# Performance work log

Hardware: AMD Instinct MI355X
Metric: run time of the kernel (lower is better)

## Reference

```python
import jax, jax.numpy as jnp
import numpy as np

D_MODEL = 2048
NUM_HEADS = 16
HEAD_DIM = D_MODEL // NUM_HEADS
SCALE = HEAD_DIM ** 0.5
B, TQ, CACHE_LEN = 4, 1024, 1024


def setup_inputs() -> dict:
    key = jax.random.key(0)
    ks = jax.random.split(key, 13)
    f = jnp.float32
    inp = {
        'query': jax.random.normal(ks[0], (B, TQ, D_MODEL), f),
        'key': jax.random.normal(ks[1], (B, TQ, D_MODEL), f),
        'value': jax.random.normal(ks[2], (B, TQ, D_MODEL), f),
        'cache_key': jax.random.normal(ks[3], (B, CACHE_LEN, D_MODEL), f),
        'cache_value': jax.random.normal(ks[4], (B, CACHE_LEN, D_MODEL), f),
        'Wq': jax.random.normal(ks[5], (D_MODEL, D_MODEL), f) * 0.02,
        'bq': jnp.zeros((D_MODEL,), f),
        'Wk': jax.random.normal(ks[6], (D_MODEL, D_MODEL), f) * 0.02,
        'bk': jnp.zeros((D_MODEL,), f),
        'Wv': jax.random.normal(ks[7], (D_MODEL, D_MODEL), f) * 0.02,
        'bv': jnp.zeros((D_MODEL,), f),
        'Wo': jax.random.normal(ks[8], (D_MODEL, D_MODEL), f) * 0.02,
        'bo': jnp.zeros((D_MODEL,), f),
    }
    return inp


def _split(x):
    b, t, _ = x.shape
    return jnp.transpose(x.reshape(b, t, NUM_HEADS, HEAD_DIM), (0, 2, 1, 3))  # [B,H,T,Dh]


def reference(query, key, value, cache_key, cache_value, Wq, bq, Wk, bk, Wv, bv, Wo, bo):
    b, tq, _ = query.shape
    Q = query @ Wq.T + bq
    K = key @ Wk.T + bk
    V = value @ Wv.T + bv
    # cache holds already-projected K/V; concat along time
    K = jnp.concatenate([cache_key, K], axis=1)
    V = jnp.concatenate([cache_value, V], axis=1)
    total = K.shape[1]
    Qh, Kh, Vh = _split(Q), _split(K), _split(V)  # [B,H,T,Dh]
    scores = jnp.einsum('bhqd,bhkd->bhqk', Qh, Kh) / SCALE  # [B,H,Tq,total]
    # faithful to original: tril(Tq, total) mask (row i sees cols 0..i)
    mask = jnp.tril(jnp.ones((tq, total), dtype=bool))
    scores = jnp.where(mask[None, None], scores, -jnp.inf)
    attn = jax.nn.softmax(scores, axis=-1)  # eval mode: no dropout
    out = jnp.einsum('bhqk,bhkd->bhqd', attn, Vh)
    out = jnp.transpose(out, (0, 2, 1, 3)).reshape(b, tq, D_MODEL)
    out = out @ Wo.T + bo
    # new cache: torch reshapes the transposed [B,H,T,Dh] tensor directly
    new_k = Kh.reshape(b, -1, D_MODEL)
    new_v = Vh.reshape(b, -1, D_MODEL)
    return out, new_k, new_v
```

## Files before the change

### kernel.cpp

```cpp
#include <hip/hip_runtime.h>
#include <hip/hip_bf16.h>


typedef __bf16 bf16x8 __attribute__((ext_vector_type(8)));
typedef __bf16 bf16x4 __attribute__((ext_vector_type(4)));
typedef unsigned short u16x8 __attribute__((ext_vector_type(8)));
typedef float  f32x4  __attribute__((ext_vector_type(4)));
typedef unsigned int u32;

#define MFMA16(a, b, c) __builtin_amdgcn_mfma_f32_16x16x32_bf16((a), (b), (c), 0, 0, 0)

__device__ __forceinline__ void async16(__bf16* lds_p, const __bf16* g) {
    __builtin_amdgcn_global_load_lds(
        (__attribute__((address_space(1))) void*)g,
        (__attribute__((address_space(3))) void*)lds_p, 16, 0, 0);
}

__global__ __launch_bounds__(256) void prep(
    const float* __restrict__ q, const float* __restrict__ k, const float* __restrict__ v,
    const float* __restrict__ wq, const float* __restrict__ wk,
    const float* __restrict__ wv, const float* __restrict__ wo,
    const float* __restrict__ ck, const float* __restrict__ cv,
    float* __restrict__ nk, float* __restrict__ nv,
    __bf16* __restrict__ dq, __bf16* __restrict__ dk, __bf16* __restrict__ dv,
    __bf16* __restrict__ dwq, __bf16* __restrict__ dwk,
    __bf16* __restrict__ dwv, __bf16* __restrict__ dwo,
    __bf16* __restrict__ ckb, __bf16* __restrict__ cvb) {
    const int nthreads = gridDim.x * blockDim.x;
    for (int i = blockIdx.x * blockDim.x + threadIdx.x; i < 9437184; i += nthreads) {
        if (i < 4194304) {
            const int sel = i >> 21;
            const int j = i & 2097151;
            const int dh4 = j & 31;
            const int t = (j >> 5) & 1023;
            const int h = (j >> 15) & 15;
            const int b = j >> 19;
            const float* src = sel ? cv : ck;
            float* dst = sel ? nv : nk;
            __bf16* dstb = sel ? cvb : ckb;
            const size_t si = ((size_t)(b << 10) + t) * 2048 + (h << 7) + (dh4 << 2);
            const size_t di = ((size_t)b << 22) + ((size_t)h << 18) + (t << 7) + (dh4 << 2);
            const size_t bi = (((size_t)(b * 16 + h) * 1024 + t) << 7) + (dh4 << 2);
            const f32x4 x = *(const f32x4*)&src[si];
            *(f32x4*)&dst[di] = x;
            bf16x4 bx;
#pragma unroll
            for (int e = 0; e < 4; e++) bx[e] = (__bf16)x[e];
            *(bf16x4*)&dstb[bi] = bx;
        } else {
            const float* s;
            __bf16* d;
            int off;
            if (i < 7340032) {
                const int ii = i - 4194304;
                const int r = ii >> 20;
                off = ii & 1048575;
                s = (r == 0) ? q : (r == 1) ? k : v;
                d = (r == 0) ? dq : (r == 1) ? dk : dv;
            } else {
                const int ii = i - 7340032;
                const int r = ii >> 19;
                off = ii & 524287;
                s = (r == 0) ? wq : (r == 1) ? wk : (r == 2) ? wv : wo;
                d = (r == 0) ? dwq : (r == 1) ? dwk : (r == 2) ? dwv : dwo;
            }
            const f32x4 x0 = *(const f32x4*)(s + (size_t)off * 8);
            const f32x4 x1 = *(const f32x4*)(s + (size_t)off * 8 + 4);
            bf16x8 o;
#pragma unroll
            for (int j2 = 0; j2 < 4; j2++) {
                o[j2]     = (__bf16)x0[j2];
                o[j2 + 4] = (__bf16)x1[j2];
            }
            *(bf16x8*)(d + (size_t)off * 8) = o;
        }
    }
}

template <int MODE>
__global__ __launch_bounds__(512, 2) void gemm8(
    const __bf16* __restrict__ A,
    const __bf16* __restrict__ W0, const __bf16* __restrict__ W1,
    const __bf16* __restrict__ W2,
    const float* __restrict__ bz0, const float* __restrict__ bz1,
    const float* __restrict__ bz2,
    void* __restrict__ C0, float* __restrict__ C1, float* __restrict__ C2) {
    extern __shared__ __bf16 lds[];
    constexpr int K = 2048;
    const int tid = threadIdx.x;
    const int w = tid >> 6, lane = tid & 63;
    const int wm = w >> 2, wn = w & 3;
    const int g = lane >> 4, c = lane & 15;

    const int lin = blockIdx.x;
    const int nb = lin & 7, mb = lin >> 3;
    const int m0 = mb << 8, n0 = nb << 8;
    const int seg = (MODE == 1) ? (mb >> 4) : 0;
    const __bf16* W = (MODE == 0 || seg == 0) ? W0 : (seg == 1) ? W1 : W2;
    const float* bias = (MODE == 0) ? bz0 : (seg == 0) ? bz0 : (seg == 1) ? bz1 : bz2;

    const __bf16* Ab = A + (size_t)m0 * K;
    const __bf16* Wb = W + (size_t)n0 * K;

    const int sch = (lane & 3) ^ (((lane >> 5) & 1) << 1);
    const int srow = lane >> 2;
    const int foff = c * 32 + ((g ^ ((c >> 3) << 1)) << 3);
    const int arow0 = wm * 8;
    const int brow0 = wn * 4;

    f32x4 acc[8][4] = {};

    auto stg = [&](const __bf16* src, int T, int kk, int region, int bf) {
#pragma unroll
        for (int cc = 0; cc < 2; cc++) {
            const __bf16* gs = src + (size_t)((cc * 8 + w) * 16 + srow) * K
                             + T * 64 + kk * 32 + sch * 8;
            async16(&lds[bf * 32768 + region * 16384 + kk * 8192 + (cc * 8 + w) * 512], gs);
        }
    };

    stg(Ab, 0, 0, 0, 0); stg(Wb, 0, 0, 1, 0);
    stg(Ab, 0, 1, 0, 0); stg(Wb, 0, 1, 1, 0);
    stg(Ab, 1, 0, 0, 1); stg(Wb, 1, 0, 1, 1);
    stg(Ab, 1, 1, 0, 1); stg(Wb, 1, 1, 1, 1);
    asm volatile("s_waitcnt vmcnt(0)" ::: "memory");
    asm volatile("s_barrier" ::: "memory");

#pragma unroll 2
    for (int T = 0; T < 32; T++) {
        const int bf = T & 1;
        const int ab = bf * 32768;
        const int bb = bf * 32768 + 16384;
        bf16x8 fa[4], fb[4], fb2[4];

#pragma unroll
        for (int i = 0; i < 4; i++)
            fa[i] = *(const bf16x8*)&lds[ab + (arow0 + i) * 512 + foff];
#pragma unroll
        for (int j = 0; j < 4; j++)
            fb[j] = *(const bf16x8*)&lds[bb + (brow0 + j) * 512 + foff];
        if (T >= 1 && T <= 30) stg(Ab, T + 1, 1, 0, bf ^ 1);
        asm volatile("s_barrier" ::: "memory");
        asm volatile("s_waitcnt lgkmcnt(0)" ::: "memory");
        __builtin_amdgcn_sched_barrier(0);
        __builtin_amdgcn_s_setprio(1);
#pragma unroll
        for (int i = 0; i < 4; i++)
#pragma unroll
            for (int j = 0; j < 4; j++)
                acc[i][j] = MFMA16(fa[i], fb[j], acc[i][j]);
        __builtin_amdgcn_s_setprio(0);
        asm volatile("s_barrier" ::: "memory");

#pragma unroll
        for (int i = 0; i < 4; i++)
            fa[i] = *(const bf16x8*)&lds[ab + (arow0 + 4 + i) * 512 + foff];
        if (T >= 1 && T <= 30) stg(Wb, T + 1, 1, 1, bf ^ 1);
        asm volatile("s_barrier" ::: "memory");
        asm volatile("s_waitcnt lgkmcnt(0)" ::: "memory");
        __builtin_amdgcn_sched_barrier(0);
        __builtin_amdgcn_s_setprio(1);
#pragma unroll
        for (int i = 0; i < 4; i++)
#pragma unroll
            for (int j = 0; j < 4; j++)
                acc[4 + i][j] = MFMA16(fa[i], fb[j], acc[4 + i][j]);
        __builtin_amdgcn_s_setprio(0);
        asm volatile("s_barrier" ::: "memory");

#pragma unroll
        for (int i = 0; i < 4; i++)
            fa[i] = *(const bf16x8*)&lds[ab + 8192 + (arow0 + i) * 512 + foff];
#pragma unroll
        for (int j = 0; j < 4; j++)
            fb2[j] = *(const bf16x8*)&lds[bb + 8192 + (brow0 + j) * 512 + foff];
        if (T <= 29) stg(Ab, T + 2, 0, 0, bf);
        asm volatile("s_barrier" ::: "memory");
        asm volatile("s_waitcnt lgkmcnt(0)" ::: "memory");
        __builtin_amdgcn_sched_barrier(0);
        __builtin_amdgcn_s_setprio(1);
#pragma unroll
        for (int i = 0; i < 4; i++)
#pragma unroll
            for (int j = 0; j < 4; j++)
                acc[i][j] = MFMA16(fa[i], fb2[j], acc[i][j]);
        __builtin_amdgcn_s_setprio(0);
        asm volatile("s_barrier" ::: "memory");

#pragma unroll
        for (int i = 0; i < 4; i++)
            fa[i] = *(const bf16x8*)&lds[ab + 8192 + (arow0 + 4 + i) * 512 + foff];
        if (T <= 29) stg(Wb, T + 2, 0, 1, bf);
        if (T >= 30) asm volatile("s_waitcnt vmcnt(0)" ::: "memory");
        else         asm volatile("s_waitcnt vmcnt(4)" ::: "memory");
        asm volatile("s_barrier" ::: "memory");
        asm volatile("s_waitcnt lgkmcnt(0)" ::: "memory");
        __builtin_amdgcn_sched_barrier(0);
        __builtin_amdgcn_s_setprio(1);
#pragma unroll
        for (int i = 0; i < 4; i++)
#pragma unroll
            for (int j = 0; j < 4; j++)
                acc[4 + i][j] = MFMA16(fa[i], fb2[j], acc[4 + i][j]);
        __builtin_amdgcn_s_setprio(0);
        asm volatile("s_barrier" ::: "memory");
    }

#pragma unroll
    for (int mi = 0; mi < 8; mi++) {
#pragma unroll
        for (int ni = 0; ni < 4; ni++) {
            const int col = n0 + wn * 64 + ni * 16 + c;
            const float bv = bias[col];
            const int rowb = m0 + wm * 128 + mi * 16 + g * 4;
            if (MODE == 0) {
                float* Cf = (float*)C0;
#pragma unroll
                for (int r = 0; r < 4; r++)
                    Cf[(size_t)(rowb + r) * 2048 + col] = acc[mi][ni][r] + bv;
            } else {
                const int h = col >> 7, dh = col & 127;
#pragma unroll
                for (int r = 0; r < 4; r++) {
                    const float v = acc[mi][ni][r] + bv;
                    const int lrow = (rowb + r) & 4095;
                    const int b = lrow >> 10, t = lrow & 1023;
                    if (seg == 0)
                        ((__bf16*)C0)[(((size_t)(b * 16 + h) * 1024) + t) * 128 + dh] = (__bf16)v;
                    else if (seg == 1)
                        C1[(((size_t)(b * 16 + h) * 2048) + 1024 + t) * 128 + dh] = v;
                    else
                        C2[(((size_t)(b * 16 + h) * 2048) + 1024 + t) * 128 + dh] = v;
                }
            }
        }
    }
}

__global__ __launch_bounds__(256) void attn_k(const __bf16* __restrict__ Qw,
                                              const __bf16* __restrict__ cK,
                                              const __bf16* __restrict__ cV,
                                              __bf16* __restrict__ O) {
    __shared__ __bf16 Kt[32 * 128];
    __shared__ u32 Vt32[128 * 16];
    __shared__ __bf16 Pw[4][16 * 32];

    const int tid = threadIdx.x;
    const int w = tid >> 6;
    const int lane = tid & 63;
    const int g = lane >> 4, c = lane & 15;

    const int lin = blockIdx.x + (blockIdx.y << 4) + (blockIdx.z << 8);
    const int chunk = lin >> 8, idx = lin & 255;
    int qb = idx & 15;
    if (chunk & 1) qb = 15 - qb;
    const int bh = (idx >> 4) + (chunk << 4);
    const int b = bh >> 4, h = bh & 15;
    const int q0 = qb << 6;
    const float inv_scale = 0.08838834764831845f;

    const __bf16* qbase = Qw + (((size_t)(b * 16 + h) * 1024) + q0 + w * 16) * 128;
    bf16x8 qf[4];
#pragma unroll
    for (int dc = 0; dc < 4; dc++)
        qf[dc] = *(const bf16x8*)&qbase[c * 128 + dc * 32 + g * 8];

    f32x4 accO[8] = {};
    float m_run[4], l_run[4];
#pragma unroll
    for (int r = 0; r < 4; r++) { m_run[r] = -1e30f; l_run[r] = 0.0f; }

    const int trips = (q0 >> 5) + 2;
    const __bf16* kb = cK + (size_t)(b * 16 + h) * 1024 * 128;
    const __bf16* vb = cV + (size_t)(b * 16 + h) * 1024 * 128;

    const int skey = tid >> 3, sdh = (tid & 7) * 16;
    const int kp = tid >> 4, db = tid & 15;
    const int vcol = (((kp >> 2) ^ (db & 3)) << 2) | (kp & 3);

    for (int kt = 0; kt < trips; kt++) {
        const int k0 = kt * 32;
        const bf16x8 k_lo = *(const bf16x8*)&kb[(size_t)(k0 + skey) * 128 + sdh];
        const bf16x8 k_hi = *(const bf16x8*)&kb[(size_t)(k0 + skey) * 128 + sdh + 8];
        const bf16x8 v0 = *(const bf16x8*)&vb[(size_t)(k0 + 2 * kp) * 128 + db * 8];
        const bf16x8 v1 = *(const bf16x8*)&vb[(size_t)(k0 + 2 * kp + 1) * 128 + db * 8];
        __syncthreads();
        {
            const int ss = skey & 7, ch0 = (tid & 7) * 2;
            *(bf16x8*)&Kt[skey * 128 + ((ch0 ^ ss) << 3)]       = k_lo;
            *(bf16x8*)&Kt[skey * 128 + (((ch0 + 1) ^ ss) << 3)] = k_hi;
        }
        {
            const u16x8 pa = __builtin_bit_cast(u16x8, v0);
            const u16x8 pb = __builtin_bit_cast(u16x8, v1);
#pragma unroll
            for (int j = 0; j < 8; j++)
                Vt32[(db * 8 + j) * 16 + vcol] = (u32)pa[j] | ((u32)pb[j] << 16);
        }
        __syncthreads();

        f32x4 s_acc[2] = {};
#pragma unroll
        for (int nt = 0; nt < 2; nt++) {
            const int krow = nt * 16 + c;
            const int ks = krow & 7;
#pragma unroll
            for (int dc = 0; dc < 4; dc++) {
                const bf16x8 kf =
                    *(const bf16x8*)&Kt[krow * 128 + (((dc * 4 + g) ^ ks) << 3)];
                s_acc[nt] = MFMA16(qf[dc], kf, s_acc[nt]);
            }
        }

        float p[2][4], alpha[4];
#pragma unroll
        for (int r = 0; r < 4; r++) {
            const int qrow = q0 + w * 16 + g * 4 + r;
            float s0 = (k0 + c      <= qrow) ? s_acc[0][r] * inv_scale : -1e30f;
            float s1 = (k0 + 16 + c <= qrow) ? s_acc[1][r] * inv_scale : -1e30f;
            float rm = fmaxf(s0, s1);
            rm = fmaxf(rm, __shfl_xor(rm, 1));
            rm = fmaxf(rm, __shfl_xor(rm, 2));
            rm = fmaxf(rm, __shfl_xor(rm, 4));
            rm = fmaxf(rm, __shfl_xor(rm, 8));
            const float mnew = fmaxf(m_run[r], rm);
            alpha[r] = __expf(m_run[r] - mnew);
            const float p0 = __expf(s0 - mnew);
            const float p1 = __expf(s1 - mnew);
            p[0][r] = p0; p[1][r] = p1;
            float ps = p0 + p1;
            ps += __shfl_xor(ps, 1);
            ps += __shfl_xor(ps, 2);
            ps += __shfl_xor(ps, 4);
            ps += __shfl_xor(ps, 8);
            l_run[r] = alpha[r] * l_run[r] + ps;
            m_run[r] = mnew;
        }
#pragma unroll
        for (int nt2 = 0; nt2 < 8; nt2++)
#pragma unroll
            for (int r = 0; r < 4; r++)
                accO[nt2][r] *= alpha[r];

#pragma unroll
        for (int nt = 0; nt < 2; nt++)
#pragma unroll
            for (int r = 0; r < 4; r++)
                Pw[w][(g * 4 + r) * 32 + ((((nt << 1) | (c >> 3)) ^ g) << 3) + (c & 7)] =
                    (__bf16)p[nt][r];
        asm volatile("s_waitcnt lgkmcnt(0)" ::: "memory");
        __builtin_amdgcn_sched_barrier(0);

        const bf16x8 pf = *(const bf16x8*)&Pw[w][c * 32 + ((g ^ ((c >> 2) & 3)) << 3)];
#pragma unroll
        for (int nt2 = 0; nt2 < 8; nt2++) {
            const int vrow = nt2 * 16 + c;
            const bf16x8 vf = *(const bf16x8*)&(
                (const __bf16*)Vt32)[vrow * 32 + ((g ^ ((vrow >> 3) & 3)) << 3)];
            accO[nt2] = MFMA16(pf, vf, accO[nt2]);
        }
    }

#pragma unroll
    for (int nt2 = 0; nt2 < 8; nt2++)
#pragma unroll
        for (int r = 0; r < 4; r++) {
            const float v = accO[nt2][r] / l_run[r];
            const int row = b * 1024 + q0 + w * 16 + g * 4 + r;
            const int col = h * 128 + nt2 * 16 + c;
            O[(size_t)row * 2048 + col] = (__bf16)v;
        }
}

extern "C" void kernel_launch(void* const* d_in, const int* in_sizes, int n_in,
                              void* d_out, int out_size, void* d_ws, size_t ws_size,
                              hipStream_t stream) {
    const float* query       = (const float*)d_in[0];
    const float* key         = (const float*)d_in[1];
    const float* value       = (const float*)d_in[2];
    const float* cache_key   = (const float*)d_in[3];
    const float* cache_value = (const float*)d_in[4];
    const float* Wq = (const float*)d_in[5];
    const float* bq = (const float*)d_in[6];
    const float* Wk = (const float*)d_in[7];
    const float* bk = (const float*)d_in[8];
    const float* Wv = (const float*)d_in[9];
    const float* bv = (const float*)d_in[10];
    const float* Wo = (const float*)d_in[11];
    const float* bo = (const float*)d_in[12];

    float* out   = (float*)d_out;
    float* new_k = out + 8388608;
    float* new_v = out + 25165824;

    __bf16* p = (__bf16*)d_ws;
    __bf16* ws_q    = p; p += 8388608;
    __bf16* ws_attn = p; p += 8388608;
    __bf16* q_bf    = p; p += 8388608;
    __bf16* k_bf    = p; p += 8388608;
    __bf16* v_bf    = p; p += 8388608;
    __bf16* wq_bf   = p; p += 4194304;
    __bf16* wk_bf   = p; p += 4194304;
    __bf16* wv_bf   = p; p += 4194304;
    __bf16* wo_bf   = p; p += 4194304;
    __bf16* ck_bf   = p; p += 8388608;
    __bf16* cv_bf   = p;

    static bool s_attr = false;
    if (!s_attr) {
        hipFuncSetAttribute(reinterpret_cast<const void*>(&gemm8<1>),
                            hipFuncAttributeMaxDynamicSharedMemorySize, 131072);
        hipFuncSetAttribute(reinterpret_cast<const void*>(&gemm8<0>),
                            hipFuncAttributeMaxDynamicSharedMemorySize, 131072);
        s_attr = true;
    }

    prep<<<4096, 256, 0, stream>>>(query, key, value, Wq, Wk, Wv, Wo,
                                   cache_key, cache_value, new_k, new_v,
                                   q_bf, k_bf, v_bf, wq_bf, wk_bf, wv_bf, wo_bf,
                                   ck_bf, cv_bf);
    gemm8<1><<<384, 512, 131072, stream>>>(q_bf, wq_bf, wk_bf, wv_bf,
                                           bq, bk, bv, ws_q, new_k, new_v);
    attn_k<<<dim3(16, 16, 4), 256, 0, stream>>>(ws_q, ck_bf, cv_bf, ws_attn);
    gemm8<0><<<128, 512, 131072, stream>>>(ws_attn, wo_bf, nullptr, nullptr,
                                           bo, nullptr, nullptr, out, nullptr, nullptr);
}
```

Measured before the change: 640.4 us.

## Shrink GEMM tile to 128x256 with triple-buffered LDS pipeline, widen prep copies

The GEMM tile drops from 256x256 to 128x256, which doubles the grid (768 and 256 blocks) so the 256 CUs on the device are better filled. The K loop now uses a three-stage LDS ring buffer with prefetch distance two and partial vmcnt waits, in place of the previous double buffer. The cache-copy part of prep now moves 8 floats per thread instead of 4. The smaller tile lowers arithmetic intensity per block and raises LDS use to 144KB, which may limit co-residency.

```diff
diff --git a/kernel.cpp b/kernel.cpp
--- a/kernel.cpp
+++ b/kernel.cpp
@@ -3,7 +3,6 @@
 
 
 typedef __bf16 bf16x8 __attribute__((ext_vector_type(8)));
-typedef __bf16 bf16x4 __attribute__((ext_vector_type(4)));
 typedef unsigned short u16x8 __attribute__((ext_vector_type(8)));
 typedef float  f32x4  __attribute__((ext_vector_type(4)));
 typedef unsigned int u32;
@@ -27,38 +26,43 @@
     __bf16* __restrict__ dwv, __bf16* __restrict__ dwo,
     __bf16* __restrict__ ckb, __bf16* __restrict__ cvb) {
     const int nthreads = gridDim.x * blockDim.x;
-    for (int i = blockIdx.x * blockDim.x + threadIdx.x; i < 9437184; i += nthreads) {
-        if (i < 4194304) {
-            const int sel = i >> 21;
-            const int j = i & 2097151;
-            const int dh4 = j & 31;
-            const int t = (j >> 5) & 1023;
-            const int h = (j >> 15) & 15;
-            const int b = j >> 19;
+    for (int i = blockIdx.x * blockDim.x + threadIdx.x; i < 7340032; i += nthreads) {
+        if (i < 2097152) {
+            const int sel = i >> 20;
+            const int j = i & 1048575;
+            const int dh8 = j & 15;
+            const int t = (j >> 4) & 1023;
+            const int h = (j >> 14) & 15;
+            const int b = j >> 18;
             const float* src = sel ? cv : ck;
             float* dst = sel ? nv : nk;
             __bf16* dstb = sel ? cvb : ckb;
-            const size_t si = ((size_t)(b << 10) + t) * 2048 + (h << 7) + (dh4 << 2);
-            const size_t di = ((size_t)b << 22) + ((size_t)h << 18) + (t << 7) + (dh4 << 2);
-            const size_t bi = (((size_t)(b * 16 + h) * 1024 + t) << 7) + (dh4 << 2);
-            const f32x4 x = *(const f32x4*)&src[si];
-            *(f32x4*)&dst[di] = x;
-            bf16x4 bx;
-#pragma unroll
-            for (int e = 0; e < 4; e++) bx[e] = (__bf16)x[e];
-            *(bf16x4*)&dstb[bi] = bx;
+            const size_t si = ((size_t)(b << 10) + t) * 2048 + (h << 7) + (dh8 << 3);
+            const size_t di = ((size_t)b << 22) + ((size_t)h << 18) + (t << 7) + (dh8 << 3);
+            const size_t bi = (((size_t)(b * 16 + h) * 1024 + t) << 7) + (dh8 << 3);
+            const f32x4 x0 = *(const f32x4*)&src[si];
+            const f32x4 x1 = *(const f32x4*)&src[si + 4];
+            *(f32x4*)&dst[di] = x0;
+            *(f32x4*)&dst[di + 4] = x1;
+            bf16x8 bx;
+#pragma unroll
+            for (int e = 0; e < 4; e++) {
+                bx[e]     = (__bf16)x0[e];
+                bx[e + 4] = (__bf16)x1[e];
+            }
+            *(bf16x8*)&dstb[bi] = bx;
         } else {
             const float* s;
             __bf16* d;
             int off;
-            if (i < 7340032) {
-                const int ii = i - 4194304;
+            if (i < 5242880) {
+                const int ii = i - 2097152;
                 const int r = ii >> 20;
                 off = ii & 1048575;
                 s = (r == 0) ? q : (r == 1) ? k : v;
                 d = (r == 0) ? dq : (r == 1) ? dk : dv;
             } else {
-                const int ii = i - 7340032;
+                const int ii = i - 5242880;
                 const int r = ii >> 19;
                 off = ii & 524287;
                 s = (r == 0) ? wq : (r == 1) ? wk : (r == 2) ? wv : wo;
@@ -94,135 +98,107 @@
 
     const int lin = blockIdx.x;
     const int nb = lin & 7, mb = lin >> 3;
-    const int m0 = mb << 8, n0 = nb << 8;
-    const int seg = (MODE == 1) ? (mb >> 4) : 0;
+    const int m0 = mb << 7, n0 = nb << 8;
+    const int seg = (MODE == 1) ? (mb >> 5) : 0;
     const __bf16* W = (MODE == 0 || seg == 0) ? W0 : (seg == 1) ? W1 : W2;
     const float* bias = (MODE == 0) ? bz0 : (seg == 0) ? bz0 : (seg == 1) ? bz1 : bz2;
 
     const __bf16* Ab = A + (size_t)m0 * K;
     const __bf16* Wb = W + (size_t)n0 * K;
 
+    const int srow = lane >> 2;
     const int sch = (lane & 3) ^ (((lane >> 5) & 1) << 1);
-    const int srow = lane >> 2;
     const int foff = c * 32 + ((g ^ ((c >> 3) << 1)) << 3);
-    const int arow0 = wm * 8;
-    const int brow0 = wn * 4;
-
-    f32x4 acc[8][4] = {};
-
-    auto stg = [&](const __bf16* src, int T, int kk, int region, int bf) {
-#pragma unroll
-        for (int cc = 0; cc < 2; cc++) {
-            const __bf16* gs = src + (size_t)((cc * 8 + w) * 16 + srow) * K
-                             + T * 64 + kk * 32 + sch * 8;
-            async16(&lds[bf * 32768 + region * 16384 + kk * 8192 + (cc * 8 + w) * 512], gs);
+
+    f32x4 acc[4][4] = {};
+
+    auto stgA = [&](int T, int rg) {
+#pragma unroll
+        for (int u = 0; u < 2; u++) {
+            const __bf16* gs = Ab + (size_t)(w * 16 + srow) * K + T * 64 + u * 32 + sch * 8;
+            async16(&lds[rg * 24576 + (w * 2 + u) * 512], gs);
         }
     };
-
-    stg(Ab, 0, 0, 0, 0); stg(Wb, 0, 0, 1, 0);
-    stg(Ab, 0, 1, 0, 0); stg(Wb, 0, 1, 1, 0);
-    stg(Ab, 1, 0, 0, 1); stg(Wb, 1, 0, 1, 1);
-    stg(Ab, 1, 1, 0, 1); stg(Wb, 1, 1, 1, 1);
-    asm volatile("s_waitcnt vmcnt(0)" ::: "memory");
+    auto stgB = [&](int T, int rg) {
+#pragma unroll
+        for (int u = 0; u < 4; u++) {
+            const int rowblk = 2 * w + (u >> 1), kk = u & 1;
+            const __bf16* gs = Wb + (size_t)(rowblk * 16 + srow) * K + T * 64 + kk * 32 + sch * 8;
+            async16(&lds[rg * 24576 + 8192 + (w * 4 + u) * 512], gs);
+        }
+    };
+
+    stgA(0, 0); stgB(0, 0);
+    stgA(1, 1); stgB(1, 1);
+    asm volatile("s_waitcnt vmcnt(6)" ::: "memory");
     asm volatile("s_barrier" ::: "memory");
 
-#pragma unroll 2
+    int rg = 0;
     for (int T = 0; T < 32; T++) {
-        const int bf = T & 1;
-        const int ab = bf * 32768;
-        const int bb = bf * 32768 + 16384;
-        bf16x8 fa[4], fb[4], fb2[4];
-
-#pragma unroll
-        for (int i = 0; i < 4; i++)
-            fa[i] = *(const bf16x8*)&lds[ab + (arow0 + i) * 512 + foff];
-#pragma unroll
-        for (int j = 0; j < 4; j++)
-            fb[j] = *(const bf16x8*)&lds[bb + (brow0 + j) * 512 + foff];
-        if (T >= 1 && T <= 30) stg(Ab, T + 1, 1, 0, bf ^ 1);
+        int rs = rg + 2; if (rs >= 3) rs -= 3;
+        const int base = rg * 24576;
+        bf16x8 fa[4], fb[4];
+
+#pragma unroll
+        for (int mi = 0; mi < 4; mi++)
+            fa[mi] = *(const bf16x8*)&lds[base + ((wm * 4 + mi) * 2 + 0) * 512 + foff];
+#pragma unroll
+        for (int ni = 0; ni < 4; ni++)
+            fb[ni] = *(const bf16x8*)&lds[base + 8192 + ((wn * 4 + ni) * 2 + 0) * 512 + foff];
+        if (T < 30) stgA(T + 2, rs);
         asm volatile("s_barrier" ::: "memory");
         asm volatile("s_waitcnt lgkmcnt(0)" ::: "memory");
         __builtin_amdgcn_sched_barrier(0);
         __builtin_amdgcn_s_setprio(1);
 #pragma unroll
-        for (int i = 0; i < 4; i++)
-#pragma unroll
-            for (int j = 0; j < 4; j++)
-                acc[i][j] = MFMA16(fa[i], fb[j], acc[i][j]);
+        for (int mi = 0; mi < 4; mi++)
+#pragma unroll
+            for (int ni = 0; ni < 4; ni++)
+                acc[mi][ni] = MFMA16(fa[mi], fb[ni], acc[mi][ni]);
         __builtin_amdgcn_s_setprio(0);
         asm volatile("s_barrier" ::: "memory");
 
 #pragma unroll
-        for (int i = 0; i < 4; i++)
-            fa[i] = *(const bf16x8*)&lds[ab + (arow0 + 4 + i) * 512 + foff];
-        if (T >= 1 && T <= 30) stg(Wb, T + 1, 1, 1, bf ^ 1);
+        for (int mi = 0; mi < 4; mi++)
+            fa[mi] = *(const bf16x8*)&lds[base + ((wm * 4 + mi) * 2 + 1) * 512 + foff];
+#pragma unroll
+        for (int ni = 0; ni < 4; ni++)
+            fb[ni] = *(const bf16x8*)&lds[base + 8192 + ((wn * 4 + ni) * 2 + 1) * 512 + foff];
+        if (T < 30) {
+            stgB(T + 2, rs);
+            asm volatile("s_waitcnt vmcnt(6)" ::: "memory");
+        } else {
+            asm volatile("s_waitcnt vmcnt(0)" ::: "memory");
+        }
         asm volatile("s_barrier" ::: "memory");
         asm volatile("s_waitcnt lgkmcnt(0)" ::: "memory");
         __builtin_amdgcn_sched_barrier(0);
         __builtin_amdgcn_s_setprio(1);
 #pragma unroll
-        for (int i = 0; i < 4; i++)
-#pragma unroll
-            for (int j = 0; j < 4; j++)
-                acc[4 + i][j] = MFMA16(fa[i], fb[j], acc[4 + i][j]);
+        for (int mi = 0; mi < 4; mi++)
+#pragma unroll
+            for (int ni = 0; ni < 4; ni++)
+                acc[mi][ni] = MFMA16(fa[mi], fb[ni], acc[mi][ni]);
         __builtin_amdgcn_s_setprio(0);
         asm volatile("s_barrier" ::: "memory");
 
-#pragma unroll
-        for (int i = 0; i < 4; i++)
-            fa[i] = *(const bf16x8*)&lds[ab + 8192 + (arow0 + i) * 512 + foff];
-#pragma unroll
-        for (int j = 0; j < 4; j++)
-            fb2[j] = *(const bf16x8*)&lds[bb + 8192 + (brow0 + j) * 512 + foff];
-        if (T <= 29) stg(Ab, T + 2, 0, 0, bf);
-        asm volatile("s_barrier" ::: "memory");
-        asm volatile("s_waitcnt lgkmcnt(0)" ::: "memory");
-        __builtin_amdgcn_sched_barrier(0);
-        __builtin_amdgcn_s_setprio(1);
-#pragma unroll
-        for (int i = 0; i < 4; i++)
-#pragma unroll
-            for (int j = 0; j < 4; j++)
-                acc[i][j] = MFMA16(fa[i], fb2[j], acc[i][j]);
-        __builtin_amdgcn_s_setprio(0);
-        asm volatile("s_barrier" ::: "memory");
-
-#pragma unroll
-        for (int i = 0; i < 4; i++)
-            fa[i] = *(const bf16x8*)&lds[ab + 8192 + (arow0 + 4 + i) * 512 + foff];
-        if (T <= 29) stg(Wb, T + 2, 0, 1, bf);
-        if (T >= 30) asm volatile("s_waitcnt vmcnt(0)" ::: "memory");
-        else         asm volatile("s_waitcnt vmcnt(4)" ::: "memory");
-        asm volatile("s_barrier" ::: "memory");
-        asm volatile("s_waitcnt lgkmcnt(0)" ::: "memory");
-        __builtin_amdgcn_sched_barrier(0);
-        __builtin_amdgcn_s_setprio(1);
-#pragma unroll
-        for (int i = 0; i < 4; i++)
-#pragma unroll
-            for (int j = 0; j < 4; j++)
-                acc[4 + i][j] = MFMA16(fa[i], fb2[j], acc[4 + i][j]);
-        __builtin_amdgcn_s_setprio(0);
-        asm volatile("s_barrier" ::: "memory");
+        rg = (rg + 1 == 3) ? 0 : rg + 1;
     }
 
 #pragma unroll
-    for (int mi = 0; mi < 8; mi++) {
-#pragma unroll
-        for (int ni = 0; ni < 4; ni++) {
-            const int col = n0 + wn * 64 + ni * 16 + c;
-            const float bv = bias[col];
-            const int rowb = m0 + wm * 128 + mi * 16 + g * 4;
-            if (MODE == 0) {
-                float* Cf = (float*)C0;
-#pragma unroll
-                for (int r = 0; r < 4; r++)
-                    Cf[(size_t)(rowb + r) * 2048 + col] = acc[mi][ni][r] + bv;
-            } else {
-                const int h = col >> 7, dh = col & 127;
-#pragma unroll
-                for (int r = 0; r < 4; r++) {
-                    const float v = acc[mi][ni][r] + bv;
+    for (int ni = 0; ni < 4; ni++) {
+        const int col = n0 + wn * 64 + ni * 16 + c;
+        const float bv = bias[col];
+        const int h = col >> 7, dh = col & 127;
+#pragma unroll
+        for (int mi = 0; mi < 4; mi++) {
+            const int rowb = m0 + wm * 64 + mi * 16 + g * 4;
+#pragma unroll
+            for (int r = 0; r < 4; r++) {
+                const float v = acc[mi][ni][r] + bv;
+                if (MODE == 0) {
+                    ((float*)C0)[(size_t)(rowb + r) * 2048 + col] = v;
+                } else {
                     const int lrow = (rowb + r) & 4095;
                     const int b = lrow >> 10, t = lrow & 1023;
                     if (seg == 0)
@@ -409,9 +385,9 @@
     static bool s_attr = false;
     if (!s_attr) {
         hipFuncSetAttribute(reinterpret_cast<const void*>(&gemm8<1>),
-                            hipFuncAttributeMaxDynamicSharedMemorySize, 131072);
+                            hipFuncAttributeMaxDynamicSharedMemorySize, 147456);
         hipFuncSetAttribute(reinterpret_cast<const void*>(&gemm8<0>),
-                            hipFuncAttributeMaxDynamicSharedMemorySize, 131072);
+                            hipFuncAttributeMaxDynamicSharedMemorySize, 147456);
         s_attr = true;
     }
 
@@ -419,9 +395,9 @@
                                    cache_key, cache_value, new_k, new_v,
                                    q_bf, k_bf, v_bf, wq_bf, wk_bf, wv_bf, wo_bf,
                                    ck_bf, cv_bf);
-    gemm8<1><<<384, 512, 131072, stream>>>(q_bf, wq_bf, wk_bf, wv_bf,
+    gemm8<1><<<768, 512, 147456, stream>>>(q_bf, wq_bf, wk_bf, wv_bf,
                                            bq, bk, bv, ws_q, new_k, new_v);
     attn_k<<<dim3(16, 16, 4), 256, 0, stream>>>(ws_q, ck_bf, cv_bf, ws_attn);
-    gemm8<0><<<128, 512, 131072, stream>>>(ws_attn, wo_bf, nullptr, nullptr,
+    gemm8<0><<<256, 512, 147456, stream>>>(ws_attn, wo_bf, nullptr, nullptr,
                                            bo, nullptr, nullptr, out, nullptr, nullptr);
 }
```

Result: faster. 618.4 us (-3.4%).

## Split attention into 32-row blocks with XCD-aware mapping; widen prep and GEMM waits

Applied to the files above, without the earlier changes.

The attention kernel moves from 64-query blocks of 4 waves to 32-query blocks of 2 waves, doubling the grid. Block-to-(batch,head,qblock) assignment is remapped so each XCD handles a fixed set of heads, and causal load is balanced by pairing early and late query blocks. K/V staging now loads 32 bytes per row per thread, the prep kernel handles 8 elements per thread for the cache transpose, and the GEMM waitcnt threshold is relaxed. Smaller blocks improve load balance and L2 locality, at the cost of less K/V reuse per block staged in LDS.

```diff
diff --git a/kernel.cpp b/kernel.cpp
--- a/kernel.cpp
+++ b/kernel.cpp
@@ -3,7 +3,6 @@
 
 
 typedef __bf16 bf16x8 __attribute__((ext_vector_type(8)));
-typedef __bf16 bf16x4 __attribute__((ext_vector_type(4)));
 typedef unsigned short u16x8 __attribute__((ext_vector_type(8)));
 typedef float  f32x4  __attribute__((ext_vector_type(4)));
 typedef unsigned int u32;
@@ -27,38 +26,43 @@
     __bf16* __restrict__ dwv, __bf16* __restrict__ dwo,
     __bf16* __restrict__ ckb, __bf16* __restrict__ cvb) {
     const int nthreads = gridDim.x * blockDim.x;
-    for (int i = blockIdx.x * blockDim.x + threadIdx.x; i < 9437184; i += nthreads) {
-        if (i < 4194304) {
-            const int sel = i >> 21;
-            const int j = i & 2097151;
-            const int dh4 = j & 31;
-            const int t = (j >> 5) & 1023;
-            const int h = (j >> 15) & 15;
-            const int b = j >> 19;
+    for (int i = blockIdx.x * blockDim.x + threadIdx.x; i < 7340032; i += nthreads) {
+        if (i < 2097152) {
+            const int sel = i >> 20;
+            const int j = i & 1048575;
+            const int dh8 = j & 15;
+            const int t = (j >> 4) & 1023;
+            const int h = (j >> 14) & 15;
+            const int b = j >> 18;
             const float* src = sel ? cv : ck;
             float* dst = sel ? nv : nk;
             __bf16* dstb = sel ? cvb : ckb;
-            const size_t si = ((size_t)(b << 10) + t) * 2048 + (h << 7) + (dh4 << 2);
-            const size_t di = ((size_t)b << 22) + ((size_t)h << 18) + (t << 7) + (dh4 << 2);
-            const size_t bi = (((size_t)(b * 16 + h) * 1024 + t) << 7) + (dh4 << 2);
-            const f32x4 x = *(const f32x4*)&src[si];
-            *(f32x4*)&dst[di] = x;
-            bf16x4 bx;
-#pragma unroll
-            for (int e = 0; e < 4; e++) bx[e] = (__bf16)x[e];
-            *(bf16x4*)&dstb[bi] = bx;
+            const size_t si = ((size_t)(b << 10) + t) * 2048 + (h << 7) + (dh8 << 3);
+            const size_t di = ((size_t)b << 22) + ((size_t)h << 18) + (t << 7) + (dh8 << 3);
+            const size_t bi = (((size_t)(b * 16 + h) * 1024 + t) << 7) + (dh8 << 3);
+            const f32x4 x0 = *(const f32x4*)&src[si];
+            const f32x4 x1 = *(const f32x4*)&src[si + 4];
+            *(f32x4*)&dst[di] = x0;
+            *(f32x4*)&dst[di + 4] = x1;
+            bf16x8 bx;
+#pragma unroll
+            for (int e = 0; e < 4; e++) {
+                bx[e]     = (__bf16)x0[e];
+                bx[e + 4] = (__bf16)x1[e];
+            }
+            *(bf16x8*)&dstb[bi] = bx;
         } else {
             const float* s;
             __bf16* d;
             int off;
-            if (i < 7340032) {
-                const int ii = i - 4194304;
+            if (i < 5242880) {
+                const int ii = i - 2097152;
                 const int r = ii >> 20;
                 off = ii & 1048575;
                 s = (r == 0) ? q : (r == 1) ? k : v;
                 d = (r == 0) ? dq : (r == 1) ? dk : dv;
             } else {
-                const int ii = i - 7340032;
+                const int ii = i - 5242880;
                 const int r = ii >> 19;
                 off = ii & 524287;
                 s = (r == 0) ? wq : (r == 1) ? wk : (r == 2) ? wv : wo;
@@ -192,7 +196,7 @@
             fa[i] = *(const bf16x8*)&lds[ab + 8192 + (arow0 + 4 + i) * 512 + foff];
         if (T <= 29) stg(Wb, T + 2, 0, 1, bf);
         if (T >= 30) asm volatile("s_waitcnt vmcnt(0)" ::: "memory");
-        else         asm volatile("s_waitcnt vmcnt(4)" ::: "memory");
+        else         asm volatile("s_waitcnt vmcnt(6)" ::: "memory");
         asm volatile("s_barrier" ::: "memory");
         asm volatile("s_waitcnt lgkmcnt(0)" ::: "memory");
         __builtin_amdgcn_sched_barrier(0);
@@ -237,13 +241,13 @@
     }
 }
 
-__global__ __launch_bounds__(256) void attn_k(const __bf16* __restrict__ Qw,
+__global__ __launch_bounds__(128) void attn_k(const __bf16* __restrict__ Qw,
                                               const __bf16* __restrict__ cK,
                                               const __bf16* __restrict__ cV,
                                               __bf16* __restrict__ O) {
     __shared__ __bf16 Kt[32 * 128];
     __shared__ u32 Vt32[128 * 16];
-    __shared__ __bf16 Pw[4][16 * 32];
+    __shared__ __bf16 Pw[2][16 * 32];
 
     const int tid = threadIdx.x;
     const int w = tid >> 6;
@@ -251,15 +255,17 @@
     const int g = lane >> 4, c = lane & 15;
 
     const int lin = blockIdx.x + (blockIdx.y << 4) + (blockIdx.z << 8);
-    const int chunk = lin >> 8, idx = lin & 255;
-    int qb = idx & 15;
-    if (chunk & 1) qb = 15 - qb;
-    const int bh = (idx >> 4) + (chunk << 4);
+    const int xcd = lin & 7;
+    const int j = lin >> 3;
+    const int bh = xcd * 8 + (j & 7);
+    const int qq = j >> 3;
+    const int c4 = qq & 3, m = qq >> 2;
+    const int qb = ((m & 1) == 0) ? (c4 * 4 + (m >> 1)) : (31 - c4 * 4 - (m >> 1));
     const int b = bh >> 4, h = bh & 15;
-    const int q0 = qb << 6;
+    const int q0 = qb << 5;
     const float inv_scale = 0.08838834764831845f;
 
-    const __bf16* qbase = Qw + (((size_t)(b * 16 + h) * 1024) + q0 + w * 16) * 128;
+    const __bf16* qbase = Qw + (((size_t)bh * 1024) + q0 + w * 16) * 128;
     bf16x8 qf[4];
 #pragma unroll
     for (int dc = 0; dc < 4; dc++)
@@ -270,32 +276,49 @@
 #pragma unroll
     for (int r = 0; r < 4; r++) { m_run[r] = -1e30f; l_run[r] = 0.0f; }
 
-    const int trips = (q0 >> 5) + 2;
-    const __bf16* kb = cK + (size_t)(b * 16 + h) * 1024 * 128;
-    const __bf16* vb = cV + (size_t)(b * 16 + h) * 1024 * 128;
-
-    const int skey = tid >> 3, sdh = (tid & 7) * 16;
-    const int kp = tid >> 4, db = tid & 15;
-    const int vcol = (((kp >> 2) ^ (db & 3)) << 2) | (kp & 3);
+    const int trips = qb + 1;
+    const __bf16* kb = cK + (size_t)bh * 1024 * 128;
+    const __bf16* vb = cV + (size_t)bh * 1024 * 128;
+
+    const int skey = tid >> 2, sgrp = tid & 3;
+    const int ss = skey & 7;
+    const int kp = tid >> 3, dbv = tid & 7;
 
     for (int kt = 0; kt < trips; kt++) {
         const int k0 = kt * 32;
-        const bf16x8 k_lo = *(const bf16x8*)&kb[(size_t)(k0 + skey) * 128 + sdh];
-        const bf16x8 k_hi = *(const bf16x8*)&kb[(size_t)(k0 + skey) * 128 + sdh + 8];
-        const bf16x8 v0 = *(const bf16x8*)&vb[(size_t)(k0 + 2 * kp) * 128 + db * 8];
-        const bf16x8 v1 = *(const bf16x8*)&vb[(size_t)(k0 + 2 * kp + 1) * 128 + db * 8];
+        const __bf16* kr = &kb[(size_t)(k0 + skey) * 128 + sgrp * 32];
+        const bf16x8 k_a = *(const bf16x8*)&kr[0];
+        const bf16x8 k_b = *(const bf16x8*)&kr[8];
+        const bf16x8 k_c = *(const bf16x8*)&kr[16];
+        const bf16x8 k_d = *(const bf16x8*)&kr[24];
+        const __bf16* vr0 = &vb[(size_t)(k0 + 2 * kp) * 128 + dbv * 16];
+        const __bf16* vr1 = &vb[(size_t)(k0 + 2 * kp + 1) * 128 + dbv * 16];
+        const bf16x8 v0a = *(const bf16x8*)&vr0[0];
+        const bf16x8 v0b = *(const bf16x8*)&vr0[8];
+        const bf16x8 v1a = *(const bf16x8*)&vr1[0];
+        const bf16x8 v1b = *(const bf16x8*)&vr1[8];
         __syncthreads();
         {
-            const int ss = skey & 7, ch0 = (tid & 7) * 2;
-            *(bf16x8*)&Kt[skey * 128 + ((ch0 ^ ss) << 3)]       = k_lo;
-            *(bf16x8*)&Kt[skey * 128 + (((ch0 + 1) ^ ss) << 3)] = k_hi;
+            const int c0 = sgrp * 4;
+            *(bf16x8*)&Kt[skey * 128 + (((c0 + 0) ^ ss) << 3)] = k_a;
+            *(bf16x8*)&Kt[skey * 128 + (((c0 + 1) ^ ss) << 3)] = k_b;
+            *(bf16x8*)&Kt[skey * 128 + (((c0 + 2) ^ ss) << 3)] = k_c;
+            *(bf16x8*)&Kt[skey * 128 + (((c0 + 3) ^ ss) << 3)] = k_d;
         }
         {
-            const u16x8 pa = __builtin_bit_cast(u16x8, v0);
-            const u16x8 pb = __builtin_bit_cast(u16x8, v1);
-#pragma unroll
-            for (int j = 0; j < 8; j++)
-                Vt32[(db * 8 + j) * 16 + vcol] = (u32)pa[j] | ((u32)pb[j] << 16);
+            const u16x8 a0 = __builtin_bit_cast(u16x8, v0a);
+            const u16x8 a1 = __builtin_bit_cast(u16x8, v0b);
+            const u16x8 b0 = __builtin_bit_cast(u16x8, v1a);
+            const u16x8 b1 = __builtin_bit_cast(u16x8, v1b);
+#pragma unroll
+            for (int jj = 0; jj < 8; jj++) {
+                const int d0 = dbv * 16 + jj;
+                const int d1 = dbv * 16 + 8 + jj;
+                const int pc0 = (((kp >> 2) ^ ((d0 >> 3) & 3)) << 2) | (kp & 3);
+                const int pc1 = (((kp >> 2) ^ ((d1 >> 3) & 3)) << 2) | (kp & 3);
+                Vt32[d0 * 16 + pc0] = (u32)a0[jj] | ((u32)b0[jj] << 16);
+                Vt32[d1 * 16 + pc1] = (u32)a1[jj] | ((u32)b1[jj] << 16);
+            }
         }
         __syncthreads();
 
@@ -421,7 +444,7 @@
                                    ck_bf, cv_bf);
     gemm8<1><<<384, 512, 131072, stream>>>(q_bf, wq_bf, wk_bf, wv_bf,
                                            bq, bk, bv, ws_q, new_k, new_v);
-    attn_k<<<dim3(16, 16, 4), 256, 0, stream>>>(ws_q, ck_bf, cv_bf, ws_attn);
+    attn_k<<<dim3(16, 16, 8), 128, 0, stream>>>(ws_q, ck_bf, cv_bf, ws_attn);
     gemm8<0><<<128, 512, 131072, stream>>>(ws_attn, wo_bf, nullptr, nullptr,
                                            bo, nullptr, nullptr, out, nullptr, nullptr);
 }
```

Measured after the change: 635.3 us. Within noise of the previous version (-0.8%).
